# Optimization experiments

Measured on AMD Instinct MI355X. Metric: run time of the kernel, lower is better.

The kernel has to match this reference:

```python
import jax, jax.numpy as jnp
import numpy as np

D = 1024        # input_dim
H = 4096        # hidden_dim (expert FFN width)
RH = H // 2     # router hidden
E = 8           # expert_count
TOP_K = 2
N = 4096        # tokens
LN_EPS = 1e-5


def setup_inputs() -> dict:
    key = jax.random.key(0)
    ks = jax.random.split(key, 12)
    s_d = 1.0 / np.sqrt(D)
    s_h = 1.0 / np.sqrt(H)
    s_rh = 1.0 / np.sqrt(RH)
    return {
        "x": jax.random.normal(ks[0], (N, D), jnp.float32),
        "ln_g": jnp.ones((D,), jnp.float32),
        "ln_b": jnp.zeros((D,), jnp.float32),
        # router: Linear(D, RH) -> ReLU -> Linear(RH, E)
        "rw1": jax.random.uniform(ks[1], (D, RH), jnp.float32, -s_d, s_d),
        "rb1": jax.random.uniform(ks[2], (RH,), jnp.float32, -s_d, s_d),
        "rw2": jax.random.uniform(ks[3], (RH, E), jnp.float32, -s_rh, s_rh),
        "rb2": jax.random.uniform(ks[4], (E,), jnp.float32, -s_rh, s_rh),
        # experts: E x (Linear(D, H) -> ReLU -> Linear(H, D)); dropout is identity in eval
        "ew1": jax.random.uniform(ks[5], (E, D, H), jnp.float32, -s_d, s_d),
        "eb1": jax.random.uniform(ks[6], (E, H), jnp.float32, -s_d, s_d),
        "ew2": jax.random.uniform(ks[7], (E, H, D), jnp.float32, -s_h, s_h),
        "eb2": jax.random.uniform(ks[8], (E, D), jnp.float32, -s_h, s_h),
    }


def reference(x, ln_g, ln_b, rw1, rb1, rw2, rb2, ew1, eb1, ew2, eb2):
    residual = x
    # LayerNorm
    mu = jnp.mean(x, axis=-1, keepdims=True)
    var = jnp.mean(jnp.square(x - mu), axis=-1, keepdims=True)
    xn = (x - mu) * jax.lax.rsqrt(var + LN_EPS) * ln_g + ln_b
    # Router MLP + softmax + top-k with renormalized gates
    logits = jax.nn.relu(xn @ rw1 + rb1) @ rw2 + rb2          # [N, E]
    probs = jax.nn.softmax(logits, axis=-1)
    vals, idx = jax.lax.top_k(probs, TOP_K)                    # [N, K]
    vals = vals / jnp.sum(vals, axis=-1, keepdims=True)
    # combine weights per expert: [N, E]
    combine = jnp.sum(jax.nn.one_hot(idx, E, dtype=vals.dtype) * vals[..., None], axis=1)
    # dense grouped expert FFN: h [E, N, H], y [E, N, D]
    h = jax.nn.relu(jnp.einsum("nd,edh->enh", xn, ew1) + eb1[:, None, :])
    y = jnp.einsum("enh,ehd->end", h, ew2) + eb2[:, None, :]
    out = residual + jnp.einsum("end,ne->nd", y, combine)
    return out
```

## Files before the change

kernel.cpp:

```cpp
#include <hip/hip_runtime.h>
#include <stdint.h>

#define D_    1024
#define H_    4096
#define RH_   2048
#define E_    8
#define N_    4096
#define NK_   8192
#define MT_MAX 71
#define DELTA_MARGIN 1e-4f
#define FIX_CAP 256

typedef __bf16 bf16x8 __attribute__((ext_vector_type(8)));
typedef float  f32x4  __attribute__((ext_vector_type(4)));


__device__ __forceinline__ unsigned short f2bf(float f) {
  union { float f; unsigned u; } v; v.f = f;
  unsigned r = v.u + 0x7fffu + ((v.u >> 16) & 1u);
  return (unsigned short)(r >> 16);
}
__device__ __forceinline__ float bf2f(unsigned short h) {
  union { unsigned u; float f; } v; v.u = ((unsigned)h) << 16;
  return v.f;
}

#define GLOAD16(gp, lp) \
  __builtin_amdgcn_global_load_lds((__attribute__((address_space(1))) void*)(void*)(gp), \
                                   (__attribute__((address_space(3))) void*)(lp), 16, 0, 0)

__global__ __launch_bounds__(256) void k_transpose(const float* __restrict__ in,
                                                   unsigned short* __restrict__ outH,
                                                   unsigned short* __restrict__ outL,
                                                   int R, int C) {
  __shared__ float t[32][33];
  const int b = blockIdx.z;
  const int c0 = blockIdx.x * 32, r0 = blockIdx.y * 32;
  const int lx = threadIdx.x & 31, ly = threadIdx.x >> 5;
  const long inB = (long)R * C;
  #pragma unroll
  for (int i = 0; i < 4; i++) {
    int r = r0 + ly + i * 8;
    t[ly + i * 8][lx] = in[b * inB + (long)r * C + c0 + lx];
  }
  __syncthreads();
  #pragma unroll
  for (int i = 0; i < 4; i++) {
    int c = c0 + ly + i * 8;
    float v = t[lx][ly + i * 8];
    unsigned short h = f2bf(v);
    long oi = b * inB + (long)c * R + r0 + lx;
    outH[oi] = h;
    if (outL) outL[oi] = f2bf(v - bf2f(h));
  }
}

__global__ __launch_bounds__(256) void k_layernorm(const float* __restrict__ x,
                                                   const float* __restrict__ g,
                                                   const float* __restrict__ b,
                                                   unsigned short* __restrict__ xnh,
                                                   unsigned short* __restrict__ xnl) {
  __shared__ float red[4];
  const int n = blockIdx.x, tid = threadIdx.x;
  float4 v = ((const float4*)(x + (long)n * D_))[tid];
  float s = v.x + v.y + v.z + v.w;
  #pragma unroll
  for (int o = 32; o >= 1; o >>= 1) s += __shfl_xor(s, o, 64);
  if ((tid & 63) == 0) red[tid >> 6] = s;
  __syncthreads();
  float mean = (red[0] + red[1] + red[2] + red[3]) * (1.f / D_);
  __syncthreads();
  float d0 = v.x - mean, d1 = v.y - mean, d2 = v.z - mean, d3 = v.w - mean;
  float ss = d0 * d0 + d1 * d1 + d2 * d2 + d3 * d3;
  #pragma unroll
  for (int o = 32; o >= 1; o >>= 1) ss += __shfl_xor(ss, o, 64);
  if ((tid & 63) == 0) red[tid >> 6] = ss;
  __syncthreads();
  float rstd = rsqrtf((red[0] + red[1] + red[2] + red[3]) * (1.f / D_) + 1e-5f);
  float4 gg = ((const float4*)g)[tid];
  float4 bb = ((const float4*)b)[tid];
  float xn0 = d0 * rstd * gg.x + bb.x;
  float xn1 = d1 * rstd * gg.y + bb.y;
  float xn2 = d2 * rstd * gg.z + bb.z;
  float xn3 = d3 * rstd * gg.w + bb.w;
  unsigned short h0 = f2bf(xn0), h1 = f2bf(xn1), h2 = f2bf(xn2), h3 = f2bf(xn3);
  ((ushort4*)xnh)[(long)n * 256 + tid] = make_ushort4(h0, h1, h2, h3);
  ((ushort4*)xnl)[(long)n * 256 + tid] = make_ushort4(
      f2bf(xn0 - bf2f(h0)), f2bf(xn1 - bf2f(h1)),
      f2bf(xn2 - bf2f(h2)), f2bf(xn3 - bf2f(h3)));
}

__global__ void k_init(int* ctl) { if (threadIdx.x < 36) ctl[threadIdx.x] = 0; }

__global__ __launch_bounds__(256) void k_router_gemm(const unsigned short* __restrict__ xh,
                                                     const unsigned short* __restrict__ xl,
                                                     const unsigned short* __restrict__ bhT,
                                                     const unsigned short* __restrict__ blT,
                                                     const float* __restrict__ rb1,
                                                     float* __restrict__ h_r) {
  __shared__ __align__(16) unsigned short Ah[128 * 32], Al[128 * 32], Bh[128 * 32], Bl[128 * 32];
  const int tid = threadIdx.x, lane = tid & 63, wid = tid >> 6;
  const int m0 = blockIdx.x * 128, n0 = blockIdx.y * 128;
  const int wm = wid >> 1, wn = wid & 1;
  const int seg0 = wid * 2;
  const int srow = lane >> 2;
  const int scol = (lane & 3) * 8;
  const long a0 = (long)(m0 + seg0 * 16 + srow) * D_ + scol;
  const long a1 = a0 + 16 * D_;
  const long b0 = (long)(n0 + seg0 * 16 + srow) * D_ + scol;
  const long b1 = b0 + 16 * D_;
  const int rl = lane & 15, kh8 = (lane >> 4) * 8;
  f32x4 acc[4][4];
  #pragma unroll
  for (int i = 0; i < 4; i++)
    #pragma unroll
    for (int j = 0; j < 4; j++) acc[i][j] = 0.f;

  for (int k0 = 0; k0 < D_; k0 += 32) {
    GLOAD16(xh + a0 + k0, Ah + seg0 * 512);
    GLOAD16(xh + a1 + k0, Ah + seg0 * 512 + 512);
    GLOAD16(xl + a0 + k0, Al + seg0 * 512);
    GLOAD16(xl + a1 + k0, Al + seg0 * 512 + 512);
    GLOAD16(bhT + b0 + k0, Bh + seg0 * 512);
    GLOAD16(bhT + b1 + k0, Bh + seg0 * 512 + 512);
    GLOAD16(blT + b0 + k0, Bl + seg0 * 512);
    GLOAD16(blT + b1 + k0, Bl + seg0 * 512 + 512);
    __syncthreads();
    bf16x8 bhf[4], blf[4];
    #pragma unroll
    for (int ni = 0; ni < 4; ni++) {
      int r = (wn * 64 + ni * 16 + rl) * 32 + kh8;
      bhf[ni] = *(const bf16x8*)(Bh + r);
      blf[ni] = *(const bf16x8*)(Bl + r);
    }
    #pragma unroll
    for (int mi = 0; mi < 4; mi++) {
      int r = (wm * 64 + mi * 16 + rl) * 32 + kh8;
      bf16x8 ah = *(const bf16x8*)(Ah + r);
      bf16x8 al = *(const bf16x8*)(Al + r);
      #pragma unroll
      for (int ni = 0; ni < 4; ni++) {
        acc[mi][ni] = __builtin_amdgcn_mfma_f32_16x16x32_bf16(ah, bhf[ni], acc[mi][ni], 0, 0, 0);
        acc[mi][ni] = __builtin_amdgcn_mfma_f32_16x16x32_bf16(ah, blf[ni], acc[mi][ni], 0, 0, 0);
        acc[mi][ni] = __builtin_amdgcn_mfma_f32_16x16x32_bf16(al, bhf[ni], acc[mi][ni], 0, 0, 0);
      }
    }
    __syncthreads();
  }
  const int rg4 = (lane >> 4) * 4;
  #pragma unroll
  for (int ni = 0; ni < 4; ni++) {
    int col = n0 + wn * 64 + ni * 16 + rl;
    float bias = rb1[col];
    #pragma unroll
    for (int mi = 0; mi < 4; mi++) {
      int row = m0 + wm * 64 + mi * 16 + rg4;
      #pragma unroll
      for (int r = 0; r < 4; r++) {
        float v = acc[mi][ni][r] + bias;
        h_r[(long)(row + r) * RH_ + col] = v > 0.f ? v : 0.f;
      }
    }
  }
}

__global__ __launch_bounds__(256) void k_logits_top2(const float* __restrict__ h_r,
                                                     const float* __restrict__ rw2,
                                                     const float* __restrict__ rb2,
                                                     int* __restrict__ sel, float* __restrict__ gate,
                                                     int* __restrict__ marked, int* __restrict__ mcount) {
  const int lane = threadIdx.x & 63, wid = threadIdx.x >> 6;
  const int n = blockIdx.x * 4 + wid;
  float p[8] = {0, 0, 0, 0, 0, 0, 0, 0};
  const float* hr = h_r + (long)n * RH_;
  for (int i = 0; i < RH_ / 64; i++) {
    int c = i * 64 + lane;
    float v = hr[c];
    float4 wa = ((const float4*)(rw2 + c * 8))[0];
    float4 wb = ((const float4*)(rw2 + c * 8))[1];
    p[0] += v * wa.x; p[1] += v * wa.y; p[2] += v * wa.z; p[3] += v * wa.w;
    p[4] += v * wb.x; p[5] += v * wb.y; p[6] += v * wb.z; p[7] += v * wb.w;
  }
  #pragma unroll
  for (int e = 0; e < 8; e++)
    #pragma unroll
    for (int s = 32; s >= 1; s >>= 1) p[e] += __shfl_xor(p[e], s, 64);
  if (lane == 0) {
    float l1 = -1e30f, l2 = -1e30f, l3 = -1e30f; int e1 = 0, e2 = 0;
    #pragma unroll
    for (int e = 0; e < 8; e++) {
      float v = p[e] + rb2[e];
      if (v > l1)      { l3 = l2; l2 = l1; e2 = e1; l1 = v; e1 = e; }
      else if (v > l2) { l3 = l2; l2 = v; e2 = e; }
      else if (v > l3) { l3 = v; }
    }
    float g1 = 1.f / (1.f + expf(l2 - l1));
    sel[n * 2] = e1; sel[n * 2 + 1] = e2;
    gate[n * 2] = g1; gate[n * 2 + 1] = 1.f - g1;
    if (l2 - l3 < DELTA_MARGIN) { int i = atomicAdd(mcount, 1); marked[i] = n; }
  }
}

__global__ __launch_bounds__(256) void k_fixup1(const float* __restrict__ x,
                                                const float* __restrict__ ln_g, const float* __restrict__ ln_b,
                                                const float* __restrict__ rw1, const float* __restrict__ rb1,
                                                const int* __restrict__ marked, const int* __restrict__ mcount,
                                                double* __restrict__ hsbuf) {
  __shared__ float xs[D_];
  __shared__ float redf[4];
  __shared__ double part[64][5];
  const int tid = threadIdx.x;
  int cnt = *mcount; if (cnt > FIX_CAP) cnt = FIX_CAP;
  const int blkTok = blockIdx.x >> 5;
  const int chunk  = blockIdx.x & 31;
  for (int mi = blkTok; mi < cnt; mi += FIX_CAP) {
    const int n = marked[mi];
    float4 v = ((const float4*)(x + (long)n * D_))[tid];
    float s = v.x + v.y + v.z + v.w;
    #pragma unroll
    for (int o = 32; o >= 1; o >>= 1) s += __shfl_xor(s, o, 64);
    if ((tid & 63) == 0) redf[tid >> 6] = s;
    __syncthreads();
    float mean = (redf[0] + redf[1] + redf[2] + redf[3]) * (1.f / D_);
    __syncthreads();
    float d0 = v.x - mean, d1 = v.y - mean, d2 = v.z - mean, d3 = v.w - mean;
    float ss = d0 * d0 + d1 * d1 + d2 * d2 + d3 * d3;
    #pragma unroll
    for (int o = 32; o >= 1; o >>= 1) ss += __shfl_xor(ss, o, 64);
    if ((tid & 63) == 0) redf[tid >> 6] = ss;
    __syncthreads();
    float rstd = rsqrtf((redf[0] + redf[1] + redf[2] + redf[3]) * (1.f / D_) + 1e-5f);
    float4 gg = ((const float4*)ln_g)[tid];
    float4 bb = ((const float4*)ln_b)[tid];
    xs[tid * 4 + 0] = d0 * rstd * gg.x + bb.x;
    xs[tid * 4 + 1] = d1 * rstd * gg.y + bb.y;
    xs[tid * 4 + 2] = d2 * rstd * gg.z + bb.z;
    xs[tid * 4 + 3] = d3 * rstd * gg.w + bb.w;
    __syncthreads();
    const int lcol = tid & 63, prt = tid >> 6;
    const int col = chunk * 64 + lcol;
    const float* rp = rw1 + (long)(prt * 256) * RH_ + col;
    const float* xp = xs + prt * 256;
    double a0 = 0, a1 = 0, a2 = 0, a3 = 0;
    #pragma unroll 4
    for (int d = 0; d < 256; d += 4) {
      float w0 = rp[(long)(d + 0) * RH_];
      float w1 = rp[(long)(d + 1) * RH_];
      float w2 = rp[(long)(d + 2) * RH_];
      float w3 = rp[(long)(d + 3) * RH_];
      a0 += (double)xp[d + 0] * (double)w0;
      a1 += (double)xp[d + 1] * (double)w1;
      a2 += (double)xp[d + 2] * (double)w2;
      a3 += (double)xp[d + 3] * (double)w3;
    }
    part[lcol][prt] = (a0 + a1) + (a2 + a3);
    __syncthreads();
    if (tid < 64) {
      double a = (part[tid][0] + part[tid][1]) + (part[tid][2] + part[tid][3])
               + (double)rb1[chunk * 64 + tid];
      hsbuf[(long)mi * RH_ + chunk * 64 + tid] = a > 0.0 ? a : 0.0;
    }
    __syncthreads();
  }
}

__global__ __launch_bounds__(256) void k_fixup2(const double* __restrict__ hsbuf,
                                                const float* __restrict__ rw2, const float* __restrict__ rb2,
                                                const int* __restrict__ marked, const int* __restrict__ mcount,
                                                int* __restrict__ sel, float* __restrict__ gate) {
  __shared__ double red2[256];
  const int tid = threadIdx.x;
  int cnt = *mcount; if (cnt > FIX_CAP) cnt = FIX_CAP;
  for (int mi = blockIdx.x; mi < cnt; mi += gridDim.x) {
    const int n = marked[mi];
    const double* hs = hsbuf + (long)mi * RH_;
    const int e = tid & 7, ch = tid >> 3;
    double pp = 0.0;
    for (int c = ch * 64; c < ch * 64 + 64; c++) pp += hs[c] * (double)rw2[c * 8 + e];
    red2[tid] = pp;
    __syncthreads();
    if (tid < 128) red2[tid] += red2[tid + 128];
    __syncthreads();
    if (tid < 64) red2[tid] += red2[tid + 64];
    __syncthreads();
    if (tid < 32) red2[tid] += red2[tid + 32];
    __syncthreads();
    if (tid < 16) red2[tid] += red2[tid + 16];
    __syncthreads();
    if (tid < 8) red2[tid] += red2[tid + 8];
    __syncthreads();
    if (tid == 0) {
      double l1 = -1e300, l2 = -1e300; int e1 = 0, e2 = 0;
      for (int ee = 0; ee < 8; ee++) {
        double vv = red2[ee] + (double)rb2[ee];
        if (vv > l1)      { l2 = l1; e2 = e1; l1 = vv; e1 = ee; }
        else if (vv > l2) { l2 = vv; e2 = ee; }
      }
      double g1 = 1.0 / (1.0 + exp(l2 - l1));
      sel[n * 2] = e1; sel[n * 2 + 1] = e2;
      gate[n * 2] = (float)g1; gate[n * 2 + 1] = (float)(1.0 - g1);
    }
    __syncthreads();
  }
}

__global__ void k_count(const int* __restrict__ sel, int* ctl) {
  int n = blockIdx.x * 256 + threadIdx.x;
  if (n >= N_) return;
  atomicAdd(&ctl[sel[n * 2]], 1);
  atomicAdd(&ctl[sel[n * 2 + 1]], 1);
}
__global__ void k_offsets(int* ctl) {
  if (threadIdx.x == 0 && blockIdx.x == 0) {
    int t = 0, tt = 0;
    for (int e = 0; e < 8; e++) {
      ctl[8 + e] = t; ctl[17 + e] = tt; ctl[26 + e] = t;
      t += ctl[e]; tt += (ctl[e] + 127) >> 7;
    }
    ctl[16] = t; ctl[25] = tt;
  }
}
__global__ void k_scatter(const int* __restrict__ sel, int* ctl,
                          int* __restrict__ perm, int* __restrict__ pos) {
  int n = blockIdx.x * 256 + threadIdx.x;
  if (n >= N_) return;
  #pragma unroll
  for (int k = 0; k < 2; k++) {
    int e = sel[n * 2 + k];
    int p = atomicAdd(&ctl[26 + e], 1);
    perm[p] = n;
    pos[n * 2 + k] = p;
  }
}

template <int KD, bool GATHER, bool RELU_BF16, bool MTFAST>
__global__ __launch_bounds__(256) void k_gemm_expert(const unsigned short* __restrict__ A,
                                                     const unsigned short* __restrict__ BT,
                                                     const float* __restrict__ bias,
                                                     const int* __restrict__ ctl,
                                                     const int* __restrict__ perm,
                                                     unsigned short* __restrict__ outBF,
                                                     float* __restrict__ outF32, int NB) {
  const int* cnt = ctl; const int* off = ctl + 8; const int* toff = ctl + 17;
  const int NX = gridDim.x, MT = gridDim.y;
  const int nwg = NX * MT;
  const int F = blockIdx.y * NX + blockIdx.x;
  const int q = nwg >> 3, r8 = nwg & 7;
  const int xcd = F & 7, j = F >> 3;
  const int L = (xcd < r8 ? xcd * (q + 1) : r8 * (q + 1) + (xcd - r8) * q) + j;
  int mt, nt;
  if (MTFAST) { mt = L % MT; nt = L / MT; }
  else        { nt = L % NX; mt = L / NX; }
  if (mt >= toff[8]) return;
  int e = 0;
  #pragma unroll
  for (int i = 0; i < 7; i++) if (toff[i + 1] <= mt) e = i + 1;
  const int ltile = mt - toff[e];
  const int g0 = off[e] + ltile * 128;
  int vrows = cnt[e] - ltile * 128; if (vrows > 128) vrows = 128;
  const int n0 = nt * 128;

  __shared__ __align__(16) unsigned short At[128 * 32], Bt[128 * 32];
  __shared__ int pidx[128];
  const int tid = threadIdx.x, lane = tid & 63, wid = tid >> 6;
  if constexpr (GATHER) {
    if (tid < 128) {
      int g = g0 + tid, gmax = off[e] + cnt[e] - 1;
      pidx[tid] = perm[g <= gmax ? g : gmax];
    }
    __syncthreads();
  }
  const int seg0 = wid * 2;
  const int srow0 = seg0 * 16 + (lane >> 2);
  const int scol = (lane & 3) * 8;
  long ab0, ab1;
  if constexpr (GATHER) {
    ab0 = (long)pidx[srow0] * KD + scol;
    ab1 = (long)pidx[srow0 + 16] * KD + scol;
  } else {
    ab0 = (long)(g0 + srow0) * KD + scol;
    ab1 = ab0 + (long)16 * KD;
  }
  const long bbase = (long)e * NB * KD;
  const long bb0 = bbase + (long)(n0 + srow0) * KD + scol;
  const long bb1 = bb0 + (long)16 * KD;

  const int wm = wid >> 1, wn = wid & 1;
  const int rl = lane & 15, kh8 = (lane >> 4) * 8;
  f32x4 acc[4][4];
  #pragma unroll
  for (int i = 0; i < 4; i++)
    #pragma unroll
    for (int jj = 0; jj < 4; jj++) acc[i][jj] = 0.f;

  for (int k0 = 0; k0 < KD; k0 += 32) {
    GLOAD16(A + ab0 + k0, At + seg0 * 512);
    GLOAD16(A + ab1 + k0, At + seg0 * 512 + 512);
    GLOAD16(BT + bb0 + k0, Bt + seg0 * 512);
    GLOAD16(BT + bb1 + k0, Bt + seg0 * 512 + 512);
    __syncthreads();
    bf16x8 bfr[4];
    #pragma unroll
    for (int ni = 0; ni < 4; ni++)
      bfr[ni] = *(const bf16x8*)(Bt + (wn * 64 + ni * 16 + rl) * 32 + kh8);
    #pragma unroll
    for (int mi = 0; mi < 4; mi++) {
      bf16x8 af = *(const bf16x8*)(At + (wm * 64 + mi * 16 + rl) * 32 + kh8);
      #pragma unroll
      for (int ni = 0; ni < 4; ni++)
        acc[mi][ni] = __builtin_amdgcn_mfma_f32_16x16x32_bf16(af, bfr[ni], acc[mi][ni], 0, 0, 0);
    }
    __syncthreads();
  }
  const int rg4 = (lane >> 4) * 4;
  #pragma unroll
  for (int ni = 0; ni < 4; ni++) {
    int col = n0 + wn * 64 + ni * 16 + rl;
    float bv = bias[(long)e * NB + col];
    #pragma unroll
    for (int mi = 0; mi < 4; mi++) {
      int lrow = wm * 64 + mi * 16 + rg4;
      #pragma unroll
      for (int r = 0; r < 4; r++) {
        if (lrow + r < vrows) {
          float v = acc[mi][ni][r] + bv;
          long idx = (long)(g0 + lrow + r) * NB + col;
          if constexpr (RELU_BF16) outBF[idx] = f2bf(v > 0.f ? v : 0.f);
          else outF32[idx] = v;
        }
      }
    }
  }
}

__global__ __launch_bounds__(256) void k_combine(const float* __restrict__ x,
                                                 const float* __restrict__ y_buf,
                                                 const int* __restrict__ pos,
                                                 const float* __restrict__ gate,
                                                 float* __restrict__ out) {
  const int n = blockIdx.x, t = threadIdx.x;
  const float g0 = gate[n * 2], g1 = gate[n * 2 + 1];
  const long p0 = pos[n * 2], p1 = pos[n * 2 + 1];
  float4 xv = ((const float4*)(x + (long)n * D_))[t];
  float4 a = ((const float4*)(y_buf + p0 * D_))[t];
  float4 b = ((const float4*)(y_buf + p1 * D_))[t];
  float4 o;
  o.x = xv.x + g0 * a.x + g1 * b.x;
  o.y = xv.y + g0 * a.y + g1 * b.y;
  o.z = xv.z + g0 * a.z + g1 * b.z;
  o.w = xv.w + g0 * a.w + g1 * b.w;
  ((float4*)(out + (long)n * D_))[t] = o;
}

extern "C" void kernel_launch(void* const* d_in, const int* in_sizes, int n_in,
                              void* d_out, int out_size, void* d_ws, size_t ws_size,
                              hipStream_t stream) {
  const float* x    = (const float*)d_in[0];
  const float* ln_g = (const float*)d_in[1];
  const float* ln_b = (const float*)d_in[2];
  const float* rw1  = (const float*)d_in[3];
  const float* rb1  = (const float*)d_in[4];
  const float* rw2  = (const float*)d_in[5];
  const float* rb2  = (const float*)d_in[6];
  const float* ew1  = (const float*)d_in[7];
  const float* eb1  = (const float*)d_in[8];
  const float* ew2  = (const float*)d_in[9];
  const float* eb2  = (const float*)d_in[10];
  float* out = (float*)d_out;

  char* w = (char*)d_ws;
  size_t off = 0;
  auto alloc = [&](size_t bytes) -> char* {
    char* p = w + off;
    off += (bytes + 255) & ~(size_t)255;
    return p;
  };
  unsigned short* ew1T  = (unsigned short*)alloc((size_t)E_ * H_ * D_ * 2);
  unsigned short* ew2T  = (unsigned short*)alloc((size_t)E_ * D_ * H_ * 2);
  unsigned short* rw1hT = (unsigned short*)alloc((size_t)RH_ * D_ * 2);
  unsigned short* rw1lT = (unsigned short*)alloc((size_t)RH_ * D_ * 2);
  unsigned short* xnh   = (unsigned short*)alloc((size_t)N_ * D_ * 2);
  unsigned short* xnl   = (unsigned short*)alloc((size_t)N_ * D_ * 2);
  float*          h_r   = (float*)alloc((size_t)N_ * RH_ * 4);
  unsigned short* h_buf = (unsigned short*)alloc((size_t)(NK_ + 128) * H_ * 2);
  float*          y_buf = (float*)alloc((size_t)(NK_ + 128) * D_ * 4);
  double*         hsbuf = (double*)alloc((size_t)FIX_CAP * RH_ * 8);
  int*   sel    = (int*)alloc((size_t)N_ * 2 * 4);
  float* gate   = (float*)alloc((size_t)N_ * 2 * 4);
  int*   marked = (int*)alloc((size_t)N_ * 4);
  int*   perm   = (int*)alloc((size_t)NK_ * 4);
  int*   pos    = (int*)alloc((size_t)N_ * 2 * 4);
  int*   ctl    = (int*)alloc(64 * 4);

  k_transpose<<<dim3(H_ / 32, D_ / 32, E_), 256, 0, stream>>>(ew1, ew1T, nullptr, D_, H_);
  k_transpose<<<dim3(D_ / 32, H_ / 32, E_), 256, 0, stream>>>(ew2, ew2T, nullptr, H_, D_);
  k_transpose<<<dim3(RH_ / 32, D_ / 32, 1), 256, 0, stream>>>(rw1, rw1hT, rw1lT, D_, RH_);
  k_layernorm<<<N_, 256, 0, stream>>>(x, ln_g, ln_b, xnh, xnl);
  k_init<<<1, 64, 0, stream>>>(ctl);
  k_router_gemm<<<dim3(N_ / 128, RH_ / 128), 256, 0, stream>>>(xnh, xnl, rw1hT, rw1lT, rb1, h_r);
  k_logits_top2<<<N_ / 4, 256, 0, stream>>>(h_r, rw2, rb2, sel, gate, marked, ctl + 34);
  k_fixup1<<<FIX_CAP * 32, 256, 0, stream>>>(x, ln_g, ln_b, rw1, rb1, marked, ctl + 34, hsbuf);
  k_fixup2<<<64, 256, 0, stream>>>(hsbuf, rw2, rb2, marked, ctl + 34, sel, gate);
  k_count<<<N_ / 256, 256, 0, stream>>>(sel, ctl);
  k_offsets<<<1, 1, 0, stream>>>(ctl);
  k_scatter<<<N_ / 256, 256, 0, stream>>>(sel, ctl, perm, pos);
  k_gemm_expert<D_, true, true, true><<<dim3(H_ / 128, MT_MAX), 256, 0, stream>>>(
      xnh, ew1T, eb1, ctl, perm, h_buf, nullptr, H_);
  k_gemm_expert<H_, false, false, false><<<dim3(D_ / 128, MT_MAX), 256, 0, stream>>>(
      h_buf, ew2T, eb2, ctl, perm, nullptr, y_buf, D_);
  k_combine<<<N_, 256, 0, stream>>>(x, y_buf, pos, gate, out);

  (void)in_sizes; (void)n_in; (void)out_size; (void)ws_size;
}
```

Measured before the change: 532.5 us.

## Double-buffer expert GEMM LDS tiles with K=64 steps and XOR swizzle

Rewrites the grouped expert GEMM main loop to use two LDS buffers, so the global-to-LDS loads for the next K slice are issued while MFMAs run on the current one. It also doubles the K step to 64, which halves the number of barriers, and applies an XOR swizzle to the LDS layout to avoid bank conflicts. Gather indices now come straight from perm rather than through a shared pidx array. LDS use grows to 64 KB per block, which may cut occupancy.

```diff
diff --git a/kernel.cpp b/kernel.cpp
--- a/kernel.cpp
+++ b/kernel.cpp
@@ -334,13 +334,13 @@
 }
 
 template <int KD, bool GATHER, bool RELU_BF16, bool MTFAST>
-__global__ __launch_bounds__(256) void k_gemm_expert(const unsigned short* __restrict__ A,
-                                                     const unsigned short* __restrict__ BT,
-                                                     const float* __restrict__ bias,
-                                                     const int* __restrict__ ctl,
-                                                     const int* __restrict__ perm,
-                                                     unsigned short* __restrict__ outBF,
-                                                     float* __restrict__ outF32, int NB) {
+__global__ __launch_bounds__(256) void k_gemm_expert4(const unsigned short* __restrict__ A,
+                                                      const unsigned short* __restrict__ BT,
+                                                      const float* __restrict__ bias,
+                                                      const int* __restrict__ ctl,
+                                                      const int* __restrict__ perm,
+                                                      unsigned short* __restrict__ outBF,
+                                                      float* __restrict__ outF32, int NB) {
   const int* cnt = ctl; const int* off = ctl + 8; const int* toff = ctl + 17;
   const int NX = gridDim.x, MT = gridDim.y;
   const int nwg = NX * MT;
@@ -360,58 +360,80 @@
   int vrows = cnt[e] - ltile * 128; if (vrows > 128) vrows = 128;
   const int n0 = nt * 128;
 
-  __shared__ __align__(16) unsigned short At[128 * 32], Bt[128 * 32];
-  __shared__ int pidx[128];
+  __shared__ __align__(16) unsigned short At[2][128 * 64];
+  __shared__ __align__(16) unsigned short Bt[2][128 * 64];
   const int tid = threadIdx.x, lane = tid & 63, wid = tid >> 6;
-  if constexpr (GATHER) {
-    if (tid < 128) {
-      int g = g0 + tid, gmax = off[e] + cnt[e] - 1;
-      pidx[tid] = perm[g <= gmax ? g : gmax];
-    }
-    __syncthreads();
-  }
-  const int seg0 = wid * 2;
-  const int srow0 = seg0 * 16 + (lane >> 2);
-  const int scol = (lane & 3) * 8;
-  long ab0, ab1;
-  if constexpr (GATHER) {
-    ab0 = (long)pidx[srow0] * KD + scol;
-    ab1 = (long)pidx[srow0 + 16] * KD + scol;
-  } else {
-    ab0 = (long)(g0 + srow0) * KD + scol;
-    ab1 = ab0 + (long)16 * KD;
-  }
+  const int l8 = lane >> 3, s8 = lane & 7;
+  const int ksw = (s8 ^ l8) * 8;
+
+  long aa[4], bb[4];
   const long bbase = (long)e * NB * KD;
-  const long bb0 = bbase + (long)(n0 + srow0) * KD + scol;
-  const long bb1 = bb0 + (long)16 * KD;
+  const int gmax = off[e] + cnt[e] - 1;
+  #pragma unroll
+  for (int i = 0; i < 4; i++) {
+    int row = wid * 32 + i * 8 + l8;
+    long ar;
+    if constexpr (GATHER) {
+      int g = g0 + row;
+      ar = perm[g <= gmax ? g : gmax];
+    } else {
+      ar = g0 + row;
+    }
+    aa[i] = ar * (long)KD + ksw;
+    bb[i] = bbase + (long)(n0 + row) * KD + ksw;
+  }
 
   const int wm = wid >> 1, wn = wid & 1;
-  const int rl = lane & 15, kh8 = (lane >> 4) * 8;
+  const int rl = lane & 15, g4 = lane >> 4;
+  int sA[2], sB[2];
+  #pragma unroll
+  for (int kk = 0; kk < 2; kk++) {
+    sA[kk] = ((kk * 4 + g4) ^ (rl & 7)) * 8;
+    sB[kk] = sA[kk];
+  }
+
   f32x4 acc[4][4];
   #pragma unroll
   for (int i = 0; i < 4; i++)
     #pragma unroll
     for (int jj = 0; jj < 4; jj++) acc[i][jj] = 0.f;
 
-  for (int k0 = 0; k0 < KD; k0 += 32) {
-    GLOAD16(A + ab0 + k0, At + seg0 * 512);
-    GLOAD16(A + ab1 + k0, At + seg0 * 512 + 512);
-    GLOAD16(BT + bb0 + k0, Bt + seg0 * 512);
-    GLOAD16(BT + bb1 + k0, Bt + seg0 * 512 + 512);
-    __syncthreads();
-    bf16x8 bfr[4];
-    #pragma unroll
-    for (int ni = 0; ni < 4; ni++)
-      bfr[ni] = *(const bf16x8*)(Bt + (wn * 64 + ni * 16 + rl) * 32 + kh8);
-    #pragma unroll
-    for (int mi = 0; mi < 4; mi++) {
-      bf16x8 af = *(const bf16x8*)(At + (wm * 64 + mi * 16 + rl) * 32 + kh8);
+  auto stage = [&](int bi, int k0) {
+    #pragma unroll
+    for (int i = 0; i < 4; i++) {
+      GLOAD16(A + aa[i] + k0, &At[bi][(wid * 32 + i * 8) * 64]);
+      GLOAD16(BT + bb[i] + k0, &Bt[bi][(wid * 32 + i * 8) * 64]);
+    }
+  };
+  auto compute = [&](int bi) {
+    #pragma unroll
+    for (int kk = 0; kk < 2; kk++) {
+      bf16x8 bfr[4];
       #pragma unroll
       for (int ni = 0; ni < 4; ni++)
-        acc[mi][ni] = __builtin_amdgcn_mfma_f32_16x16x32_bf16(af, bfr[ni], acc[mi][ni], 0, 0, 0);
-    }
-    __syncthreads();
-  }
+        bfr[ni] = *(const bf16x8*)(&Bt[bi][(wn * 64 + ni * 16 + rl) * 64 + sB[kk]]);
+      #pragma unroll
+      for (int mi = 0; mi < 4; mi++) {
+        bf16x8 af = *(const bf16x8*)(&At[bi][(wm * 64 + mi * 16 + rl) * 64 + sA[kk]]);
+        #pragma unroll
+        for (int ni = 0; ni < 4; ni++)
+          acc[mi][ni] = __builtin_amdgcn_mfma_f32_16x16x32_bf16(af, bfr[ni], acc[mi][ni], 0, 0, 0);
+      }
+    }
+  };
+
+  constexpr int NT = KD / 64;
+  stage(0, 0);
+  __syncthreads();
+  int cur = 0;
+  for (int t = 0; t < NT - 1; ++t) {
+    stage(cur ^ 1, (t + 1) * 64);
+    compute(cur);
+    __syncthreads();
+    cur ^= 1;
+  }
+  compute(cur);
+
   const int rg4 = (lane >> 4) * 4;
   #pragma unroll
   for (int ni = 0; ni < 4; ni++) {
@@ -504,9 +526,9 @@
   k_count<<<N_ / 256, 256, 0, stream>>>(sel, ctl);
   k_offsets<<<1, 1, 0, stream>>>(ctl);
   k_scatter<<<N_ / 256, 256, 0, stream>>>(sel, ctl, perm, pos);
-  k_gemm_expert<D_, true, true, true><<<dim3(H_ / 128, MT_MAX), 256, 0, stream>>>(
+  k_gemm_expert4<D_, true, true, true><<<dim3(H_ / 128, MT_MAX), 256, 0, stream>>>(
       xnh, ew1T, eb1, ctl, perm, h_buf, nullptr, H_);
-  k_gemm_expert<H_, false, false, false><<<dim3(D_ / 128, MT_MAX), 256, 0, stream>>>(
+  k_gemm_expert4<H_, false, false, false><<<dim3(D_ / 128, MT_MAX), 256, 0, stream>>>(
       h_buf, ew2T, eb2, ctl, perm, nullptr, y_buf, D_);
   k_combine<<<N_, 256, 0, stream>>>(x, y_buf, pos, gate, out);
 
```

New measurement: 617.2 us. 1.16x slower.

## Widen transpose tiles, store expert output in bf16, move weight transposes

Applied to the files above, without the earlier changes.

The weight transpose kernel now handles 64x64 tiles and writes 16 contiguous bf16 values per thread as vector stores instead of scattered 2-byte stores. The second expert GEMM writes its output in bf16 rather than fp32, which halves y_buf traffic, and the combine kernel reads bf16. The expert weight transposes are reordered to run just before their GEMMs, which may keep the freshly written transposed weights in cache. Rounding y to bf16 before combining adds some precision loss.

```diff
diff --git a/kernel.cpp b/kernel.cpp
--- a/kernel.cpp
+++ b/kernel.cpp
@@ -33,25 +33,33 @@
                                                    unsigned short* __restrict__ outH,
                                                    unsigned short* __restrict__ outL,
                                                    int R, int C) {
-  __shared__ float t[32][33];
+  __shared__ float t[64][65];
   const int b = blockIdx.z;
-  const int c0 = blockIdx.x * 32, r0 = blockIdx.y * 32;
-  const int lx = threadIdx.x & 31, ly = threadIdx.x >> 5;
+  const int c0 = blockIdx.x * 64, r0 = blockIdx.y * 64;
+  const int lx = threadIdx.x & 63, ly = threadIdx.x >> 6;
   const long inB = (long)R * C;
-  #pragma unroll
-  for (int i = 0; i < 4; i++) {
-    int r = r0 + ly + i * 8;
-    t[ly + i * 8][lx] = in[b * inB + (long)r * C + c0 + lx];
-  }
+  const float* ip = in + b * inB + (long)r0 * C + c0 + lx;
+  #pragma unroll
+  for (int i = 0; i < 16; i++)
+    t[ly + i * 4][lx] = ip[(long)(ly + i * 4) * C];
   __syncthreads();
-  #pragma unroll
-  for (int i = 0; i < 4; i++) {
-    int c = c0 + ly + i * 8;
-    float v = t[lx][ly + i * 8];
-    unsigned short h = f2bf(v);
-    long oi = b * inB + (long)c * R + r0 + lx;
-    outH[oi] = h;
-    if (outL) outL[oi] = f2bf(v - bf2f(h));
+  const int wy = threadIdx.x >> 2;
+  const int wx = (threadIdx.x & 3) * 16;
+  const int c = c0 + wy;
+  const long ob = b * inB + (long)c * R + r0 + wx;
+  unsigned short h[16];
+  #pragma unroll
+  for (int j = 0; j < 16; j++) h[j] = f2bf(t[wx + j][wy]);
+  #pragma unroll
+  for (int j = 0; j < 4; j++)
+    *(ushort4*)&outH[ob + j * 4] = make_ushort4(h[j*4], h[j*4+1], h[j*4+2], h[j*4+3]);
+  if (outL) {
+    unsigned short l[16];
+    #pragma unroll
+    for (int j = 0; j < 16; j++) l[j] = f2bf(t[wx + j][wy] - bf2f(h[j]));
+    #pragma unroll
+    for (int j = 0; j < 4; j++)
+      *(ushort4*)&outL[ob + j * 4] = make_ushort4(l[j*4], l[j*4+1], l[j*4+2], l[j*4+3]);
   }
 }
 
@@ -333,14 +341,13 @@
   }
 }
 
-template <int KD, bool GATHER, bool RELU_BF16, bool MTFAST>
+template <int KD, bool GATHER, bool RELU, bool MTFAST>
 __global__ __launch_bounds__(256) void k_gemm_expert(const unsigned short* __restrict__ A,
                                                      const unsigned short* __restrict__ BT,
                                                      const float* __restrict__ bias,
                                                      const int* __restrict__ ctl,
                                                      const int* __restrict__ perm,
-                                                     unsigned short* __restrict__ outBF,
-                                                     float* __restrict__ outF32, int NB) {
+                                                     unsigned short* __restrict__ outBF, int NB) {
   const int* cnt = ctl; const int* off = ctl + 8; const int* toff = ctl + 17;
   const int NX = gridDim.x, MT = gridDim.y;
   const int nwg = NX * MT;
@@ -425,8 +432,8 @@
         if (lrow + r < vrows) {
           float v = acc[mi][ni][r] + bv;
           long idx = (long)(g0 + lrow + r) * NB + col;
-          if constexpr (RELU_BF16) outBF[idx] = f2bf(v > 0.f ? v : 0.f);
-          else outF32[idx] = v;
+          if constexpr (RELU) outBF[idx] = f2bf(v > 0.f ? v : 0.f);
+          else                outBF[idx] = f2bf(v);
         }
       }
     }
@@ -434,7 +441,7 @@
 }
 
 __global__ __launch_bounds__(256) void k_combine(const float* __restrict__ x,
-                                                 const float* __restrict__ y_buf,
+                                                 const unsigned short* __restrict__ y_buf,
                                                  const int* __restrict__ pos,
                                                  const float* __restrict__ gate,
                                                  float* __restrict__ out) {
@@ -442,13 +449,13 @@
   const float g0 = gate[n * 2], g1 = gate[n * 2 + 1];
   const long p0 = pos[n * 2], p1 = pos[n * 2 + 1];
   float4 xv = ((const float4*)(x + (long)n * D_))[t];
-  float4 a = ((const float4*)(y_buf + p0 * D_))[t];
-  float4 b = ((const float4*)(y_buf + p1 * D_))[t];
+  ushort4 ya = ((const ushort4*)(y_buf + p0 * D_))[t];
+  ushort4 yb = ((const ushort4*)(y_buf + p1 * D_))[t];
   float4 o;
-  o.x = xv.x + g0 * a.x + g1 * b.x;
-  o.y = xv.y + g0 * a.y + g1 * b.y;
-  o.z = xv.z + g0 * a.z + g1 * b.z;
-  o.w = xv.w + g0 * a.w + g1 * b.w;
+  o.x = xv.x + g0 * bf2f(ya.x) + g1 * bf2f(yb.x);
+  o.y = xv.y + g0 * bf2f(ya.y) + g1 * bf2f(yb.y);
+  o.z = xv.z + g0 * bf2f(ya.z) + g1 * bf2f(yb.z);
+  o.w = xv.w + g0 * bf2f(ya.w) + g1 * bf2f(yb.w);
   ((float4*)(out + (long)n * D_))[t] = o;
 }
 
@@ -483,7 +490,7 @@
   unsigned short* xnl   = (unsigned short*)alloc((size_t)N_ * D_ * 2);
   float*          h_r   = (float*)alloc((size_t)N_ * RH_ * 4);
   unsigned short* h_buf = (unsigned short*)alloc((size_t)(NK_ + 128) * H_ * 2);
-  float*          y_buf = (float*)alloc((size_t)(NK_ + 128) * D_ * 4);
+  unsigned short* y_buf = (unsigned short*)alloc((size_t)(NK_ + 128) * D_ * 2);
   double*         hsbuf = (double*)alloc((size_t)FIX_CAP * RH_ * 8);
   int*   sel    = (int*)alloc((size_t)N_ * 2 * 4);
   float* gate   = (float*)alloc((size_t)N_ * 2 * 4);
@@ -492,9 +499,7 @@
   int*   pos    = (int*)alloc((size_t)N_ * 2 * 4);
   int*   ctl    = (int*)alloc(64 * 4);
 
-  k_transpose<<<dim3(H_ / 32, D_ / 32, E_), 256, 0, stream>>>(ew1, ew1T, nullptr, D_, H_);
-  k_transpose<<<dim3(D_ / 32, H_ / 32, E_), 256, 0, stream>>>(ew2, ew2T, nullptr, H_, D_);
-  k_transpose<<<dim3(RH_ / 32, D_ / 32, 1), 256, 0, stream>>>(rw1, rw1hT, rw1lT, D_, RH_);
+  k_transpose<<<dim3(RH_ / 64, D_ / 64, 1), 256, 0, stream>>>(rw1, rw1hT, rw1lT, D_, RH_);
   k_layernorm<<<N_, 256, 0, stream>>>(x, ln_g, ln_b, xnh, xnl);
   k_init<<<1, 64, 0, stream>>>(ctl);
   k_router_gemm<<<dim3(N_ / 128, RH_ / 128), 256, 0, stream>>>(xnh, xnl, rw1hT, rw1lT, rb1, h_r);
@@ -504,10 +509,12 @@
   k_count<<<N_ / 256, 256, 0, stream>>>(sel, ctl);
   k_offsets<<<1, 1, 0, stream>>>(ctl);
   k_scatter<<<N_ / 256, 256, 0, stream>>>(sel, ctl, perm, pos);
+  k_transpose<<<dim3(H_ / 64, D_ / 64, E_), 256, 0, stream>>>(ew1, ew1T, nullptr, D_, H_);
   k_gemm_expert<D_, true, true, true><<<dim3(H_ / 128, MT_MAX), 256, 0, stream>>>(
-      xnh, ew1T, eb1, ctl, perm, h_buf, nullptr, H_);
+      xnh, ew1T, eb1, ctl, perm, h_buf, H_);
+  k_transpose<<<dim3(D_ / 64, H_ / 64, E_), 256, 0, stream>>>(ew2, ew2T, nullptr, H_, D_);
   k_gemm_expert<H_, false, false, false><<<dim3(D_ / 128, MT_MAX), 256, 0, stream>>>(
-      h_buf, ew2T, eb2, ctl, perm, nullptr, y_buf, D_);
+      h_buf, ew2T, eb2, ctl, perm, y_buf, D_);
   k_combine<<<N_, 256, 0, stream>>>(x, y_buf, pos, gate, out);
 
   (void)in_sizes; (void)n_in; (void)out_size; (void)ws_size;
```

Result: no change. 525.1 us (-1.4%).
